# Performance work log

Hardware: AMD Instinct MI355X
Metric: run time of the kernel (lower is better)

Reference implementation:

```python
import jax, jax.numpy as jnp
import numpy as np

B, S, HID = 1, 2048, 2048
NH = 16
QL, KVL = 1536, 512
DN, DR, DV = 128, 64, 128
DQ = DN + DR  # 192
IH, ID = 4, 128
TOPK = 1024
EPS = 1e-6
THETA = 10000.0


def rope_interleaved(x, cos, sin):
    # x: (b,s,h,d); cos/sin: (s,d//2); pairs are (x[...,2i], x[...,2i+1])
    xr = x[..., 0::2]
    xi = x[..., 1::2]
    c = cos[None, :, None, :]
    s = sin[None, :, None, :]
    yr = xr * c - xi * s
    yi = xr * s + xi * c
    return jnp.stack([yr, yi], axis=-1).reshape(x.shape)


def rope_noninterleaved(x, cos, sin):
    # rotate-half style: pairs are (x[...,i], x[...,i+d/2])
    d = x.shape[-1] // 2
    x1, x2 = x[..., :d], x[..., d:]
    c = cos[None, :, None, :]
    s = sin[None, :, None, :]
    return jnp.concatenate([x1 * c - x2 * s, x1 * s + x2 * c], axis=-1)


def rmsnorm(x, w):
    var = jnp.mean(x * x, axis=-1, keepdims=True)
    return w * (x * jax.lax.rsqrt(var + EPS))


def layernorm(x, g, b):
    mu = jnp.mean(x, axis=-1, keepdims=True)
    var = jnp.mean((x - mu) ** 2, axis=-1, keepdims=True)
    return (x - mu) * jax.lax.rsqrt(var + EPS) * g + b


def setup_inputs() -> dict:
    key = jax.random.key(0)
    ks = jax.random.split(key, 12)
    std = 0.02
    x = jax.random.normal(ks[0], (B, S, HID), jnp.float32)
    pos = jnp.arange(S, dtype=jnp.float32)
    inv_freq = THETA ** (-jnp.arange(0, DR, 2, dtype=jnp.float32) / DR)
    ang = pos[:, None] * inv_freq[None, :]  # (S, DR//2)
    cos, sin = jnp.cos(ang), jnp.sin(ang)
    mask = jnp.where(jnp.tril(jnp.ones((S, S), bool)), 0.0, -1e9).astype(jnp.float32)
    return {
        "x": x, "cos": cos, "sin": sin, "mask": mask,
        "Wq_a": jax.random.normal(ks[1], (HID, QL), jnp.float32) * std,
        "q_norm_w": jnp.ones((QL,), jnp.float32),
        "Wq_b": jax.random.normal(ks[2], (QL, NH * DQ), jnp.float32) * std,
        "Wkv_a": jax.random.normal(ks[3], (HID, KVL + DR), jnp.float32) * std,
        "kv_norm_w": jnp.ones((KVL,), jnp.float32),
        "Wkv_b": jax.random.normal(ks[4], (KVL, NH * (DN + DV)), jnp.float32) * std,
        "Wo": jax.random.normal(ks[5], (NH * DV, HID), jnp.float32) * std,
        "IWq_b": jax.random.normal(ks[6], (QL, IH * ID), jnp.float32) * std,
        "IWk": jax.random.normal(ks[7], (HID, ID), jnp.float32) * std,
        "Ik_norm_w": jnp.ones((ID,), jnp.float32),
        "Ik_norm_b": jnp.zeros((ID,), jnp.float32),
        "IWproj": jax.random.normal(ks[8], (HID, IH), jnp.float32) * std,
    }


def indexer(x, qr, cos, sin, mask, IWq_b, IWk, Ik_norm_w, Ik_norm_b, IWproj):
    b, s, _ = x.shape
    q = (qr @ IWq_b).reshape(b, s, IH, ID)
    q_pe, q_nope = q[..., :DR], q[..., DR:]
    q_pe = rope_noninterleaved(q_pe, cos, sin)
    q = jnp.concatenate([q_pe, q_nope], axis=-1)
    k = layernorm(x @ IWk, Ik_norm_w, Ik_norm_b)  # (b,s,ID)
    k_pe = rope_noninterleaved(k[:, :, None, :DR], cos, sin)[:, :, 0]
    k = jnp.concatenate([k_pe, k[..., DR:]], axis=-1)
    weights = (x @ IWproj) * (IH ** -0.5) * (ID ** -0.5)  # (b,s,IH)
    logits = jax.nn.relu(jnp.einsum('bthd,bsd->btsh', q, k))
    index_score = jnp.einsum('btsh,bth->bts', logits, weights)
    index_score = index_score + mask[None]
    k_top = min(TOPK, s)
    topk_idx = jax.lax.top_k(index_score, k_top)[1]  # (b,s,k)
    bi = jnp.arange(b)[:, None, None]
    si = jnp.arange(s)[None, :, None]
    index_mask = jnp.full((b, s, s), -1e9, jnp.float32).at[bi, si, topk_idx].set(0.0)
    return index_mask


def reference(x, cos, sin, mask, Wq_a, q_norm_w, Wq_b, Wkv_a, kv_norm_w, Wkv_b, Wo,
              IWq_b, IWk, Ik_norm_w, Ik_norm_b, IWproj):
    b, s, _ = x.shape
    qr = rmsnorm(x @ Wq_a, q_norm_w)  # (b,s,QL)
    q = (qr @ Wq_b).reshape(b, s, NH, DQ)
    q_nope, q_pe = q[..., :DN], q[..., DN:]
    q_pe = rope_interleaved(q_pe, cos, sin)
    q = jnp.concatenate([q_nope, q_pe], axis=-1)
    kv_full = x @ Wkv_a
    kv, k_pe = kv_full[..., :KVL], kv_full[..., KVL:]
    kv = rmsnorm(kv, kv_norm_w)
    k_pe = rope_interleaved(k_pe[:, :, None, :], cos, sin)  # (b,s,1,DR)
    kv_exp = (kv @ Wkv_b).reshape(b, s, NH, DN + DV)
    k_nope, v = kv_exp[..., :DN], kv_exp[..., DN:]
    k = jnp.concatenate([k_nope, jnp.broadcast_to(k_pe, (b, s, NH, DR))], axis=-1)
    scores = jnp.einsum('bshd,bthd->bsht', q, k) * (DQ ** -0.5)
    index_mask = indexer(x, qr, cos, sin, mask, IWq_b, IWk, Ik_norm_w, Ik_norm_b, IWproj)
    scores = scores + index_mask[:, :, None, :] + mask[None, :, None, :]
    probs = jax.nn.softmax(scores, axis=-1)
    out = jnp.einsum('bsht,bthd->bshd', probs, v).reshape(b, s, NH * DV)
    return out @ Wo
```

## Files before the change

kernel.cpp:

```cpp
#include <hip/hip_runtime.h>
#include <math.h>
#include <stdint.h>

#define S 2048
#define HID 2048
#define NH 16
#define QL 1536
#define KVL 512
#define DN 128
#define DR 64
#define DV 128
#define DQ 192
#define IH 4
#define ID 128
#define TOPK 1024

#define N1 2244
#define N2 3584

#define CDIV(a,b) (((a)+(b)-1)/(b))

typedef float f32x4 __attribute__((ext_vector_type(4)));
typedef short bf16x8 __attribute__((ext_vector_type(8)));

__device__ __forceinline__ ushort f2b(float f) {
    uint32_t u = __float_as_uint(f);
    u += 0x7fffu + ((u >> 16) & 1u);
    return (ushort)(u >> 16);
}

#define GLL16(g, l)                                                            \
    __builtin_amdgcn_global_load_lds(                                          \
        (const __attribute__((address_space(1))) void*)(g),                    \
        (__attribute__((address_space(3))) void*)(l), 16, 0, 0)

__global__ __launch_bounds__(256) void gemm_bt(const ushort* __restrict__ A,
                                               const ushort* __restrict__ BT,
                                               float* __restrict__ C,
                                               int M, int N, int K) {
    __shared__ ushort As[2][128 * 32];
    __shared__ ushort Bs[2][128 * 32];
    const int tid = threadIdx.x;
    const int w = tid >> 6, l = tid & 63;
    const int quad = l >> 4, lane = l & 15;
    const int row0 = blockIdx.y * 128, col0 = blockIdx.x * 128;
    const int wr = (w >> 1) * 64, wc = (w & 1) * 64;
    f32x4 acc[4][4];
#pragma unroll
    for (int i = 0; i < 4; i++)
#pragma unroll
        for (int j = 0; j < 4; j++) acc[i][j] = (f32x4)0.f;

    const int srow = w * 32 + (l >> 2);
    const int c8 = (l & 3) * 8;
    const ushort* pa0 = A + (size_t)(row0 + srow) * K + c8;
    const ushort* pa1 = A + (size_t)(row0 + srow + 16) * K + c8;
    int bn0 = col0 + srow;      if (bn0 > N - 1) bn0 = N - 1;
    int bn1 = col0 + srow + 16; if (bn1 > N - 1) bn1 = N - 1;
    const ushort* pb0 = BT + (size_t)bn0 * K + c8;
    const ushort* pb1 = BT + (size_t)bn1 * K + c8;
    const int soff = srow * 32 + c8;

    GLL16(pa0, &As[0][soff]);
    GLL16(pa1, &As[0][soff + 16 * 32]);
    GLL16(pb0, &Bs[0][soff]);
    GLL16(pb1, &Bs[0][soff + 16 * 32]);
    asm volatile("s_waitcnt vmcnt(0)" ::: "memory");
    __builtin_amdgcn_s_barrier();

    int cur = 0;
    for (int k0 = 0; k0 < K; k0 += 32) {
        const int nxt = cur ^ 1;
        if (k0 + 32 < K) {
            GLL16(pa0 + k0 + 32, &As[nxt][soff]);
            GLL16(pa1 + k0 + 32, &As[nxt][soff + 16 * 32]);
            GLL16(pb0 + k0 + 32, &Bs[nxt][soff]);
            GLL16(pb1 + k0 + 32, &Bs[nxt][soff + 16 * 32]);
        }
        bf16x8 af[4], bf[4];
#pragma unroll
        for (int mi = 0; mi < 4; mi++)
            af[mi] = *(const bf16x8*)(&As[cur][(wr + mi * 16 + lane) * 32 + quad * 8]);
#pragma unroll
        for (int ni = 0; ni < 4; ni++)
            bf[ni] = *(const bf16x8*)(&Bs[cur][(wc + ni * 16 + lane) * 32 + quad * 8]);
#pragma unroll
        for (int mi = 0; mi < 4; mi++)
#pragma unroll
            for (int ni = 0; ni < 4; ni++)
                acc[mi][ni] = __builtin_amdgcn_mfma_f32_16x16x32_bf16(af[mi], bf[ni], acc[mi][ni], 0, 0, 0);
        asm volatile("s_waitcnt vmcnt(0)" ::: "memory");
        __builtin_amdgcn_s_barrier();
        cur = nxt;
    }
#pragma unroll
    for (int mi = 0; mi < 4; mi++)
#pragma unroll
        for (int ni = 0; ni < 4; ni++)
#pragma unroll
            for (int r = 0; r < 4; r++) {
                int row = row0 + wr + mi * 16 + quad * 4 + r;
                int col = col0 + wc + ni * 16 + lane;
                if (col < N) C[(size_t)row * N + col] = acc[mi][ni][r];
            }
}

__global__ __launch_bounds__(256) void gemm_bt_h(const ushort* __restrict__ A,
                                                 const ushort* __restrict__ BT,
                                                 ushort* __restrict__ C,
                                                 int M, int N, int K) {
    __shared__ ushort As[2][128 * 32];
    __shared__ ushort Bs[2][128 * 32];
    const int tid = threadIdx.x;
    const int w = tid >> 6, l = tid & 63;
    const int quad = l >> 4, lane = l & 15;
    const int row0 = blockIdx.y * 128, col0 = blockIdx.x * 128;
    const int wr = (w >> 1) * 64, wc = (w & 1) * 64;
    f32x4 acc[4][4];
#pragma unroll
    for (int i = 0; i < 4; i++)
#pragma unroll
        for (int j = 0; j < 4; j++) acc[i][j] = (f32x4)0.f;

    const int srow = w * 32 + (l >> 2);
    const int c8 = (l & 3) * 8;
    const ushort* pa0 = A + (size_t)(row0 + srow) * K + c8;
    const ushort* pa1 = A + (size_t)(row0 + srow + 16) * K + c8;
    int bn0 = col0 + srow;      if (bn0 > N - 1) bn0 = N - 1;
    int bn1 = col0 + srow + 16; if (bn1 > N - 1) bn1 = N - 1;
    const ushort* pb0 = BT + (size_t)bn0 * K + c8;
    const ushort* pb1 = BT + (size_t)bn1 * K + c8;
    const int soff = srow * 32 + c8;

    GLL16(pa0, &As[0][soff]);
    GLL16(pa1, &As[0][soff + 16 * 32]);
    GLL16(pb0, &Bs[0][soff]);
    GLL16(pb1, &Bs[0][soff + 16 * 32]);
    asm volatile("s_waitcnt vmcnt(0)" ::: "memory");
    __builtin_amdgcn_s_barrier();

    int cur = 0;
    for (int k0 = 0; k0 < K; k0 += 32) {
        const int nxt = cur ^ 1;
        if (k0 + 32 < K) {
            GLL16(pa0 + k0 + 32, &As[nxt][soff]);
            GLL16(pa1 + k0 + 32, &As[nxt][soff + 16 * 32]);
            GLL16(pb0 + k0 + 32, &Bs[nxt][soff]);
            GLL16(pb1 + k0 + 32, &Bs[nxt][soff + 16 * 32]);
        }
        bf16x8 af[4], bf[4];
#pragma unroll
        for (int mi = 0; mi < 4; mi++)
            af[mi] = *(const bf16x8*)(&As[cur][(wr + mi * 16 + lane) * 32 + quad * 8]);
#pragma unroll
        for (int ni = 0; ni < 4; ni++)
            bf[ni] = *(const bf16x8*)(&Bs[cur][(wc + ni * 16 + lane) * 32 + quad * 8]);
#pragma unroll
        for (int mi = 0; mi < 4; mi++)
#pragma unroll
            for (int ni = 0; ni < 4; ni++)
                acc[mi][ni] = __builtin_amdgcn_mfma_f32_16x16x32_bf16(af[mi], bf[ni], acc[mi][ni], 0, 0, 0);
        asm volatile("s_waitcnt vmcnt(0)" ::: "memory");
        __builtin_amdgcn_s_barrier();
        cur = nxt;
    }
#pragma unroll
    for (int mi = 0; mi < 4; mi++)
#pragma unroll
        for (int ni = 0; ni < 4; ni++)
#pragma unroll
            for (int r = 0; r < 4; r++) {
                int row = row0 + wr + mi * 16 + quad * 4 + r;
                int col = col0 + wc + ni * 16 + lane;
                if (col < N) C[(size_t)row * N + col] = f2b(acc[mi][ni][r]);
            }
}

__device__ __forceinline__ void wtrans_body(const float* W, ushort* WT, int K, int N,
                                            int k0, int n0) {
    __shared__ float t[64][65];
    int rr = threadIdx.x >> 6, cc = threadIdx.x & 63;
#pragma unroll
    for (int p = 0; p < 16; p++) {
        int k = k0 + p * 4 + rr, n = n0 + cc;
        t[p * 4 + rr][cc] = (k < K && n < N) ? W[(size_t)k * N + n] : 0.f;
    }
    __syncthreads();
#pragma unroll
    for (int p = 0; p < 16; p++) {
        int n = n0 + p * 4 + rr, k = k0 + cc;
        if (n < N && k < K) WT[(size_t)n * K + k] = f2b(t[cc][p * 4 + rr]);
    }
}

__global__ __launch_bounds__(256) void wtrans(const float* __restrict__ W, ushort* __restrict__ WT,
                                              int K, int N) {
    wtrans_body(W, WT, K, N, blockIdx.x * 64, blockIdx.y * 64);
}

__global__ __launch_bounds__(256) void wtrans_c1(const float* __restrict__ W0, const float* __restrict__ W1,
                                                 const float* __restrict__ W2, const float* __restrict__ W3,
                                                 ushort* __restrict__ WT) {
    int yb = blockIdx.y;
    const float* W; int N; size_t off; int y;
    if (yb < 24)      { W = W0; N = 1536; off = 0;                      y = yb; }
    else if (yb < 33) { W = W1; N = 576;  off = (size_t)1536 * HID;     y = yb - 24; }
    else if (yb < 35) { W = W2; N = 128;  off = (size_t)2112 * HID;     y = yb - 33; }
    else              { W = W3; N = 4;    off = (size_t)2240 * HID;     y = yb - 35; }
    wtrans_body(W, WT + off, HID, N, blockIdx.x * 64, y * 64);
}

__global__ __launch_bounds__(256) void wtrans_c2(const float* __restrict__ W0, const float* __restrict__ W1,
                                                 ushort* __restrict__ WT) {
    int yb = blockIdx.y;
    const float* W; int N; size_t off; int y;
    if (yb < 48) { W = W0; N = 3072; off = 0;                  y = yb; }
    else         { W = W1; N = 512;  off = (size_t)3072 * QL;  y = yb - 48; }
    wtrans_body(W, WT + off, QL, N, blockIdx.x * 64, y * 64);
}

__global__ void cvt_bf16(const float* __restrict__ in, ushort* __restrict__ out) {
    int i = blockIdx.x * 256 + threadIdx.x;
    float4 v = *(const float4*)(in + (size_t)i * 4);
    uint32_t lo = (uint32_t)f2b(v.x) | ((uint32_t)f2b(v.y) << 16);
    uint32_t hi = (uint32_t)f2b(v.z) | ((uint32_t)f2b(v.w) << 16);
    *(uint2*)(out + (size_t)i * 4) = make_uint2(lo, hi);
}

__global__ __launch_bounds__(256) void post_c1(const float* __restrict__ C1,
                                               const float* __restrict__ qw,
                                               const float* __restrict__ kvw,
                                               const float* __restrict__ ikg,
                                               const float* __restrict__ ikb,
                                               const float* __restrict__ cosb,
                                               const float* __restrict__ sinb,
                                               ushort* __restrict__ qrb,
                                               ushort* __restrict__ kvnb,
                                               float* __restrict__ kpe,
                                               float* __restrict__ kiT) {
    const int t = blockIdx.x, tid = threadIdx.x;
    const float* row = C1 + (size_t)t * N1;
    __shared__ float red[256];
    __shared__ float kis[128];
    float ss = 0.f;
    for (int i = tid; i < 1536; i += 256) { float v = row[i]; ss += v * v; }
    red[tid] = ss; __syncthreads();
    for (int st = 128; st > 0; st >>= 1) { if (tid < st) red[tid] += red[tid + st]; __syncthreads(); }
    float sq = rsqrtf(red[0] / 1536.f + 1e-6f);
    __syncthreads();
    float s2 = 0.f;
    for (int i = tid; i < 512; i += 256) { float v = row[1536 + i]; s2 += v * v; }
    red[tid] = s2; __syncthreads();
    for (int st = 128; st > 0; st >>= 1) { if (tid < st) red[tid] += red[tid + st]; __syncthreads(); }
    float skv = rsqrtf(red[0] / 512.f + 1e-6f);
    __syncthreads();
    float kv_ = (tid < 128) ? row[2112 + tid] : 0.f;
    red[tid] = kv_; __syncthreads();
    for (int st = 128; st > 0; st >>= 1) { if (tid < st) red[tid] += red[tid + st]; __syncthreads(); }
    float mu = red[0] / 128.f;
    __syncthreads();
    red[tid] = kv_ * kv_; __syncthreads();
    for (int st = 128; st > 0; st >>= 1) { if (tid < st) red[tid] += red[tid + st]; __syncthreads(); }
    float var = red[0] / 128.f - mu * mu;
    for (int i = tid; i < 1536; i += 256) qrb[(size_t)t * QL + i] = f2b(row[i] * sq * qw[i]);
    for (int i = tid; i < 512; i += 256)  kvnb[(size_t)t * KVL + i] = f2b(row[1536 + i] * skv * kvw[i]);
    if (tid < 32) {
        float c = cosb[t * 32 + tid], s = sinb[t * 32 + tid];
        float xr = row[2048 + 2 * tid], xi = row[2048 + 2 * tid + 1];
        kpe[t * 64 + 2 * tid]     = xr * c - xi * s;
        kpe[t * 64 + 2 * tid + 1] = xr * s + xi * c;
    }
    if (tid < 128) kis[tid] = (kv_ - mu) * rsqrtf(var + 1e-6f) * ikg[tid] + ikb[tid];
    __syncthreads();
    if (tid < 128) {
        float outv;
        if (tid < 32) {
            float c = cosb[t * 32 + tid], s = sinb[t * 32 + tid];
            outv = kis[tid] * c - kis[tid + 32] * s;
        } else if (tid < 64) {
            int j = tid - 32;
            float c = cosb[t * 32 + j], s = sinb[t * 32 + j];
            outv = kis[j] * s + kis[tid] * c;
        } else {
            outv = kis[tid];
        }
        kiT[(size_t)tid * S + t] = outv;
    }
}

__global__ __launch_bounds__(256) void post_c2(float* __restrict__ C2,
                                               const float* __restrict__ cosb,
                                               const float* __restrict__ sinb,
                                               ushort* __restrict__ qb) {
    const int t = blockIdx.x, tid = threadIdx.x;
    __shared__ float cs[32], sn[32];
    if (tid < 32) { cs[tid] = cosb[t * 32 + tid]; sn[tid] = sinb[t * 32 + tid]; }
    __syncthreads();
    const float sc = 0.10412775370051047f;
    const float* src0 = C2 + (size_t)t * N2;
    for (int i = tid; i < NH * 96; i += 256) {
        int h = i / 96, p = i % 96;
        const float* src = src0 + h * 192;
        ushort* dst = qb + ((size_t)h * S + t) * 192;
        if (p < 64) {
            dst[2 * p]     = f2b(src[2 * p] * sc);
            dst[2 * p + 1] = f2b(src[2 * p + 1] * sc);
        } else {
            int j = p - 64;
            float c = cs[j], s = sn[j];
            float xr = src[128 + 2 * j], xi = src[128 + 2 * j + 1];
            dst[128 + 2 * j]     = f2b((xr * c - xi * s) * sc);
            dst[128 + 2 * j + 1] = f2b((xr * s + xi * c) * sc);
        }
    }
    if (tid < 128) {
        int h = tid >> 5, j = tid & 31;
        float* p = C2 + (size_t)t * N2 + 3072 + h * 128;
        float c = cs[j], s = sn[j];
        float x1 = p[j], x2 = p[j + 32];
        p[j] = x1 * c - x2 * s;
        p[j + 32] = x1 * s + x2 * c;
    }
}

__global__ __launch_bounds__(256) void pack_kv(const ushort* __restrict__ kvexp_h,
                                               const float* __restrict__ kpe,
                                               ushort* __restrict__ kb,
                                               ushort* __restrict__ vT) {
    __shared__ ushort t[64][136];
    const int s0 = blockIdx.x * 64, h = blockIdx.y, tid = threadIdx.x;
    const int row = tid >> 2, c = tid & 3;
    const ushort* src = kvexp_h + (size_t)(s0 + row) * 4096 + h * 256;
    ushort* kbr = kb + ((size_t)h * S + s0 + row) * 192;
#pragma unroll
    for (int i = 0; i < 4; i++) {
        int off = c * 32 + i * 8;
        *(uint4*)(kbr + off) = *(const uint4*)(src + off);
        *(uint4*)(&t[row][off]) = *(const uint4*)(src + 128 + off);
    }
    const float* kp = kpe + (size_t)(s0 + row) * 64 + c * 16;
#pragma unroll
    for (int i = 0; i < 16; i++) kbr[128 + c * 16 + i] = f2b(kp[i]);
    __syncthreads();
    const int d = tid >> 1, sh = (tid & 1) * 32;
    ushort* dst = vT + ((size_t)h * 128 + d) * S + s0 + sh;
#pragma unroll
    for (int i = 0; i < 32; i++) dst[i] = t[sh + i][d];
}

__global__ __launch_bounds__(256) void iscore4(const float* __restrict__ qi,
                                               const float* __restrict__ kiT,
                                               const float* __restrict__ iw,
                                               float* __restrict__ iscore) {
    int t = blockIdx.x;
    int s0 = blockIdx.y * 1024;
    if (s0 > t) return;
    int s = s0 + threadIdx.x * 4;
    __shared__ float qs[4 * ID];
    __shared__ float ws4[4];
    for (int i = threadIdx.x; i < 4 * ID; i += 256) qs[i] = qi[(size_t)t * N2 + i];
    if (threadIdx.x < 4) ws4[threadIdx.x] = iw[(size_t)t * N1 + threadIdx.x] * 0.04419417382415922f;
    __syncthreads();
    if (s > t) return;
    float a[4][4];
#pragma unroll
    for (int h = 0; h < 4; h++)
#pragma unroll
        for (int c = 0; c < 4; c++) a[h][c] = 0.f;
    for (int d = 0; d < ID; d++) {
        float4 kv = *(const float4*)(kiT + (size_t)d * S + s);
#pragma unroll
        for (int h = 0; h < 4; h++) {
            float qv = qs[h * ID + d];
            a[h][0] += qv * kv.x; a[h][1] += qv * kv.y;
            a[h][2] += qv * kv.z; a[h][3] += qv * kv.w;
        }
    }
#pragma unroll
    for (int c = 0; c < 4; c++) {
        if (s + c > t) break;
        float sc = fmaxf(a[0][c], 0.f) * ws4[0] + fmaxf(a[1][c], 0.f) * ws4[1] +
                   fmaxf(a[2][c], 0.f) * ws4[2] + fmaxf(a[3][c], 0.f) * ws4[3];
        iscore[(size_t)t * S + s + c] = sc;
    }
}

__device__ inline unsigned sortable_u32(float f) {
    unsigned u = __float_as_uint(f);
    return (u & 0x80000000u) ? ~u : (u | 0x80000000u);
}

__global__ __launch_bounds__(256) void topk_mask(const float* __restrict__ iscore,
                                                 uint32_t* __restrict__ msk) {
    int t = blockIdx.x, tid = threadIdx.x;
    uint32_t* mrow = msk + (size_t)t * 64;
    if (t < TOPK) {
        if (tid < 64) {
            int full = (t + 1) >> 5;
            uint32_t wv2 = (tid < full) ? 0xFFFFFFFFu : 0u;
            if (tid == full) { int rem = (t + 1) & 31; wv2 = rem ? ((1u << rem) - 1u) : 0u; }
            mrow[tid] = wv2;
        }
        return;
    }
    const float* row = iscore + (size_t)t * S;
    const int n = t + 1;
    const int wv = tid >> 6;
    __shared__ int hist[4][256];
    __shared__ int scan[256];
    __shared__ int bsel, ksel;
    __shared__ uint32_t bytes[256];

    int jb = tid * 8;
    float4 v0 = *(const float4*)(row + jb);
    float4 v1 = *(const float4*)(row + jb + 4);
    uint32_t lsu[8];
    {
        float vvv[8] = {v0.x, v0.y, v0.z, v0.w, v1.x, v1.y, v1.z, v1.w};
#pragma unroll
        for (int i = 0; i < 8; i++)
            lsu[i] = (jb + i < n) ? sortable_u32(vvv[i]) : 0u;
    }
    unsigned prefix = 0, prefmask = 0;
    int k = TOPK;
    for (int pass = 0; pass < 4; pass++) {
        int shift = 24 - pass * 8;
#pragma unroll
        for (int r = 0; r < 4; r++) hist[r][tid] = 0;
        __syncthreads();
#pragma unroll
        for (int i = 0; i < 8; i++) {
            uint32_t u = lsu[i];
            if ((u & prefmask) == prefix) atomicAdd(&hist[wv][(u >> shift) & 255], 1);
        }
        __syncthreads();
        int h = hist[0][tid] + hist[1][tid] + hist[2][tid] + hist[3][tid];
        scan[tid] = h; __syncthreads();
        for (int st = 1; st < 256; st <<= 1) {
            int a = scan[tid];
            int b = (tid + st < 256) ? scan[tid + st] : 0;
            __syncthreads();
            scan[tid] = a + b;
            __syncthreads();
        }
        int snext = (tid < 255) ? scan[tid + 1] : 0;
        if (scan[tid] >= k && snext < k) { bsel = tid; ksel = k - snext; }
        __syncthreads();
        prefix |= ((unsigned)bsel) << shift;
        prefmask |= 0xFFu << shift;
        k = ksel;
        __syncthreads();
    }
    const unsigned u_thr = prefix;
    const int need = k;
    uint32_t gtbits = 0, eqbits = 0;
    int eqcnt = 0;
#pragma unroll
    for (int i = 0; i < 8; i++) {
        uint32_t u = lsu[i];
        if (u > u_thr) gtbits |= 1u << i;
        else if (u == u_thr) { eqbits |= 1u << i; eqcnt++; }
    }
    scan[tid] = eqcnt; __syncthreads();
    for (int st = 1; st < 256; st <<= 1) {
        int a = scan[tid];
        int b = (tid >= st) ? scan[tid - st] : 0;
        __syncthreads();
        scan[tid] = a + b;
        __syncthreads();
    }
    int room = need - (scan[tid] - eqcnt);
    uint32_t keep = 0;
#pragma unroll
    for (int i = 0; i < 8; i++)
        if ((eqbits >> i) & 1u) { if (room > 0) { keep |= 1u << i; room--; } }
    bytes[tid] = gtbits | keep;
    __syncthreads();
    if (tid < 64)
        mrow[tid] = bytes[tid * 4] | (bytes[tid * 4 + 1] << 8) |
                    (bytes[tid * 4 + 2] << 16) | (bytes[tid * 4 + 3] << 24);
}

__global__ __launch_bounds__(256, 2) void fattn6(const ushort* __restrict__ qb,
                                                 const ushort* __restrict__ kb,
                                                 const ushort* __restrict__ vT,
                                                 const uint32_t* __restrict__ msk,
                                                 float* __restrict__ Opart,
                                                 float* __restrict__ mlbuf) {
    __shared__ ushort Ks[24 * 512];
    __shared__ ushort Vs[16 * 512];
    __shared__ ushort Pm[4][16 * 72];
    const int tid = threadIdx.x;
    const int w = tid >> 6, l = tid & 63, quad = l >> 4, lane = l & 15;
    const int b = blockIdx.x;
    const int r8 = b & 7, j = b >> 3;
    const int h = r8 + 8 * (j & 1);
    const int idx = j >> 1;
    const int pair = idx & 15, part = idx >> 4;
    const int ta = pair, tb = 31 - pair, nA = ta + 1;
    const int vlo = part * 11, vhi = vlo + 11;
    const int qa0 = ta * 64, qb0 = tb * 64;

    bf16x8 qfa[6], qfb[6];
    {
        const ushort* qpa = qb + ((size_t)h * S + qa0 + w * 16 + lane) * 192;
        const ushort* qpb = qb + ((size_t)h * S + qb0 + w * 16 + lane) * 192;
#pragma unroll
        for (int ks = 0; ks < 6; ks++) {
            qfa[ks] = *(const bf16x8*)(qpa + ks * 32 + quad * 8);
            qfb[ks] = *(const bf16x8*)(qpb + ks * 32 + quad * 8);
        }
    }
    f32x4 oa[8], ob[8];
#pragma unroll
    for (int i = 0; i < 8; i++) { oa[i] = (f32x4)0.f; ob[i] = (f32x4)0.f; }
    float ma[4], la[4], mb[4], lb[4];
#pragma unroll
    for (int r = 0; r < 4; r++) { ma[r] = -1e30f; la[r] = 0.f; mb[r] = -1e30f; lb[r] = 0.f; }

    ushort* pw = &Pm[w][0];
    const ushort* kbase = kb + (size_t)h * S * 192;
    const ushort* vbase = vT + (size_t)h * 128 * S;

    for (int kt = 0; kt <= tb; kt++) {
        const int idxB = (kt <= ta) ? 2 * kt : kt + nA;
        const int hasA = (kt <= ta);
        const int idxA = 2 * kt + 1;
        const bool doB = (idxB >= vlo && idxB < vhi);
        const bool doA = hasA && (idxA >= vlo && idxA < vhi);
        if (!(doA || doB)) continue;
        const int s0 = kt * 64;
        __syncthreads();
#pragma unroll
        for (int ii = 0; ii < 6; ii++) {
            const int i = w * 6 + ii;
            const int ks = i >> 2, kq = i & 3;
            const ushort* src = kbase + (size_t)(s0 + kq * 16 + lane) * 192 + ks * 32 + quad * 8;
            GLL16(src, Ks + i * 512 + l * 8);
        }
#pragma unroll
        for (int ii = 0; ii < 4; ii++) {
            const int i = w * 4 + ii;
            const int k2 = i >> 3, nt = i & 7;
            const ushort* src = vbase + (size_t)(nt * 16 + lane) * S + s0 + k2 * 32 + quad * 8;
            GLL16(src, Vs + i * 512 + l * 8);
        }
        __syncthreads();

#pragma unroll
        for (int pass = 0; pass < 2; pass++) {
            if (pass == 0 && !doA) continue;
            if (pass == 1 && !doB) continue;
            const bf16x8* qf = (pass == 0) ? qfa : qfb;
            f32x4* oacc      = (pass == 0) ? oa : ob;
            float* mm        = (pass == 0) ? ma : mb;
            float* ll        = (pass == 0) ? la : lb;
            const int q0t    = (pass == 0) ? qa0 : qb0;

            f32x4 sc[4];
#pragma unroll
            for (int kq = 0; kq < 4; kq++) {
                sc[kq] = (f32x4)0.f;
#pragma unroll
                for (int ks = 0; ks < 6; ks++) {
                    bf16x8 bfr = *(const bf16x8*)(Ks + (ks * 4 + kq) * 512 + quad * 128 + lane * 8);
                    sc[kq] = __builtin_amdgcn_mfma_f32_16x16x32_bf16(qf[ks], bfr, sc[kq], 0, 0, 0);
                }
            }
            uint32_t w0[4], w1[4];
            {
                const int rowbase = q0t + w * 16 + quad * 4;
#pragma unroll
                for (int r = 0; r < 4; r++) {
                    const uint32_t* mp = msk + (size_t)(rowbase + r) * 64 + (s0 >> 5);
                    w0[r] = mp[0]; w1[r] = mp[1];
                }
            }
            float vmax[4] = {-1e30f, -1e30f, -1e30f, -1e30f};
#pragma unroll
            for (int kq = 0; kq < 4; kq++) {
                const int sh = (kq & 1) * 16 + lane;
#pragma unroll
                for (int r = 0; r < 4; r++) {
                    uint32_t word = (kq < 2) ? w0[r] : w1[r];
                    float v = ((word >> sh) & 1u) ? sc[kq][r] : -1e30f;
                    sc[kq][r] = v;
                    vmax[r] = fmaxf(vmax[r], v);
                }
            }
#pragma unroll
            for (int off = 1; off < 16; off <<= 1)
#pragma unroll
                for (int r = 0; r < 4; r++)
                    vmax[r] = fmaxf(vmax[r], __shfl_xor(vmax[r], off, 64));
            float alpha[4], psum[4];
#pragma unroll
            for (int r = 0; r < 4; r++) {
                float mnew = fmaxf(mm[r], vmax[r]);
                alpha[r] = exp2f(mm[r] - mnew);
                mm[r] = mnew;
                psum[r] = 0.f;
            }
#pragma unroll
            for (int kq = 0; kq < 4; kq++)
#pragma unroll
                for (int r = 0; r < 4; r++) {
                    float v = sc[kq][r];
                    float e = (v < -1e29f) ? 0.f : exp2f(v - mm[r]);
                    psum[r] += e;
                    pw[(quad * 4 + r) * 72 + kq * 16 + lane] = f2b(e);
                }
#pragma unroll
            for (int off = 1; off < 16; off <<= 1)
#pragma unroll
                for (int r = 0; r < 4; r++)
                    psum[r] += __shfl_xor(psum[r], off, 64);
#pragma unroll
            for (int r = 0; r < 4; r++) ll[r] = ll[r] * alpha[r] + psum[r];

            bf16x8 pfr[2];
#pragma unroll
            for (int k2 = 0; k2 < 2; k2++)
                pfr[k2] = *(const bf16x8*)(pw + lane * 72 + k2 * 32 + quad * 8);
#pragma unroll
            for (int nt = 0; nt < 8; nt++) {
#pragma unroll
                for (int r = 0; r < 4; r++) oacc[nt][r] *= alpha[r];
#pragma unroll
                for (int k2 = 0; k2 < 2; k2++) {
                    bf16x8 vfr = *(const bf16x8*)(Vs + ((k2 * 8 + nt) * 4 + quad) * 128 + lane * 8);
                    oacc[nt] = __builtin_amdgcn_mfma_f32_16x16x32_bf16(pfr[k2], vfr, oacc[nt], 0, 0, 0);
                }
            }
        }
    }
#pragma unroll
    for (int pass = 0; pass < 2; pass++) {
        const f32x4* oacc = (pass == 0) ? oa : ob;
        const float* mm   = (pass == 0) ? ma : mb;
        const float* ll   = (pass == 0) ? la : lb;
        const int qt      = (pass == 0) ? ta : tb;
        float* Op = Opart + (size_t)((qt * 16 + h) * 3 + part) * (64 * 128);
        float* mlp = mlbuf + (size_t)((qt * 16 + h) * 3 + part) * 128;
#pragma unroll
        for (int nt = 0; nt < 8; nt++)
#pragma unroll
            for (int r = 0; r < 4; r++)
                Op[(w * 16 + quad * 4 + r) * 128 + nt * 16 + lane] = oacc[nt][r];
        if (lane == 0) {
#pragma unroll
            for (int r = 0; r < 4; r++) {
                mlp[(w * 16 + quad * 4 + r) * 2 + 0] = mm[r];
                mlp[(w * 16 + quad * 4 + r) * 2 + 1] = ll[r];
            }
        }
    }
}

__global__ __launch_bounds__(256) void attn_combine(const float* __restrict__ Opart,
                                                    const float* __restrict__ mlbuf,
                                                    ushort* __restrict__ attn_b) {
    const int qt = blockIdx.x, h = blockIdx.y, tid = threadIdx.x;
    const size_t base = ((size_t)qt * 16 + h) * 3;
    const float* Op0 = Opart + base * 8192;
    const float* Op1 = Op0 + 8192;
    const float* Op2 = Op1 + 8192;
    const float* ml0 = mlbuf + base * 128;
    const float* ml1 = ml0 + 128;
    const float* ml2 = ml1 + 128;
#pragma unroll
    for (int i = 0; i < 32; i++) {
        int id = tid + i * 256;
        int row = id >> 7, d = id & 127;
        float m0 = ml0[row * 2], l0 = ml0[row * 2 + 1];
        float m1 = ml1[row * 2], l1 = ml1[row * 2 + 1];
        float m2 = ml2[row * 2], l2 = ml2[row * 2 + 1];
        float m = fmaxf(fmaxf(m0, m1), m2);
        float e0 = exp2f(m0 - m), e1 = exp2f(m1 - m), e2 = exp2f(m2 - m);
        float linv = 1.f / (l0 * e0 + l1 * e1 + l2 * e2);
        float v = (Op0[id] * e0 + Op1[id] * e1 + Op2[id] * e2) * linv;
        attn_b[(size_t)(qt * 64 + row) * 2048 + h * 128 + d] = f2b(v);
    }
}

extern "C" void kernel_launch(void* const* d_in, const int* in_sizes, int n_in,
                              void* d_out, int out_size, void* d_ws, size_t ws_size,
                              hipStream_t stream) {
    const float* x        = (const float*)d_in[0];
    const float* cosb     = (const float*)d_in[1];
    const float* sinb     = (const float*)d_in[2];
    const float* Wq_a     = (const float*)d_in[4];
    const float* q_norm_w = (const float*)d_in[5];
    const float* Wq_b     = (const float*)d_in[6];
    const float* Wkv_a    = (const float*)d_in[7];
    const float* kv_norm_w= (const float*)d_in[8];
    const float* Wkv_b    = (const float*)d_in[9];
    const float* Wo       = (const float*)d_in[10];
    const float* IWq_b    = (const float*)d_in[11];
    const float* IWk      = (const float*)d_in[12];
    const float* Ik_norm_w= (const float*)d_in[13];
    const float* Ik_norm_b= (const float*)d_in[14];
    const float* IWproj   = (const float*)d_in[15];
    float* out = (float*)d_out;

    char* ws = (char*)d_ws;
    size_t o = 0;
    auto take = [&](size_t b) { char* p = ws + o; o += (b + 255) & ~(size_t)255; return p; };
    ushort* xb     = (ushort*)take((size_t)S * HID * 2);
    ushort* qrb    = (ushort*)take((size_t)S * QL * 2);
    ushort* qb     = (ushort*)take((size_t)NH * S * DQ * 2);
    ushort* kvnb   = (ushort*)take((size_t)S * KVL * 2);
    float*  kpe    = (float*)take((size_t)S * DR * 4);
    ushort* kb     = (ushort*)take((size_t)NH * S * DQ * 2);
    ushort* vT     = (ushort*)take((size_t)NH * DV * S * 2);
    uint32_t* msk  = (uint32_t*)take((size_t)S * 64 * 4);
    float*  mlbuf  = (float*)take((size_t)32 * 16 * 3 * 64 * 2 * 4);
    ushort* WTp    = (ushort*)take((size_t)N2 * QL * 2);
    float*  C1     = (float*)take((size_t)S * N1 * 4);
    char*   big    = take((size_t)32 * 16 * 3 * 8192 * 4 + 1024);
    ushort* kvexp_h= (ushort*)take((size_t)S * 4096 * 2);
    float*  kiT    = (float*)take((size_t)128 * S * 4);
    char*   poolb  = take((size_t)16777216);

    float* C2     = (float*)big;
    float* Opart  = (float*)big;
    float* iscore = (float*)poolb;
    ushort* attn_b = (ushort*)poolb;

    cvt_bf16<<<(S * HID) / 1024, 256, 0, stream>>>(x, xb);

    wtrans_c1<<<dim3(32, 36), 256, 0, stream>>>(Wq_a, Wkv_a, IWk, IWproj, WTp);
    gemm_bt<<<dim3(CDIV(N1, 128), S / 128), 256, 0, stream>>>(xb, WTp, C1, S, N1, HID);
    post_c1<<<S, 256, 0, stream>>>(C1, q_norm_w, kv_norm_w, Ik_norm_w, Ik_norm_b,
                                   cosb, sinb, qrb, kvnb, kpe, kiT);

    wtrans_c2<<<dim3(24, 56), 256, 0, stream>>>(Wq_b, IWq_b, WTp);
    gemm_bt<<<dim3(N2 / 128, S / 128), 256, 0, stream>>>(qrb, WTp, C2, S, N2, QL);
    post_c2<<<S, 256, 0, stream>>>(C2, cosb, sinb, qb);

    wtrans<<<dim3(8, 64), 256, 0, stream>>>(Wkv_b, WTp, KVL, NH * (DN + DV));
    gemm_bt_h<<<dim3(32, S / 128), 256, 0, stream>>>(kvnb, WTp, kvexp_h, S, NH * (DN + DV), KVL);
    pack_kv<<<dim3(S / 64, NH), 256, 0, stream>>>(kvexp_h, kpe, kb, vT);

    iscore4<<<dim3(S, S / 1024), 256, 0, stream>>>(C2 + 3072, kiT, C1 + 2240, iscore);
    topk_mask<<<S, 256, 0, stream>>>(iscore, msk);

    fattn6<<<768, 256, 0, stream>>>(qb, kb, vT, msk, Opart, mlbuf);
    attn_combine<<<dim3(32, 16), 256, 0, stream>>>(Opart, mlbuf, attn_b);

    wtrans<<<dim3(32, 32), 256, 0, stream>>>(Wo, WTp, NH * DV, HID);
    gemm_bt<<<dim3(HID / 128, S / 128), 256, 0, stream>>>(attn_b, WTp, out, S, HID, NH * DV);

    (void)in_sizes; (void)n_in; (void)out_size; (void)ws_size; (void)o;
}
```

Baseline: 514.9 us.

## Load K/V fragments directly from global memory and defer row-sum reduction

The attention kernel stops staging K and V tiles through shared memory behind two block barriers per key tile. Each wave now reads its MFMA B-operand fragments straight from global memory. The cross-lane shuffle reduction of the softmax row sums moves out of the inner loop to a single pass after all tiles, which works because the per-row rescale factor is uniform across lanes. This removes the barriers and LDS traffic, but each of the four waves now fetches the full K/V tile on its own, raising cache traffic and exposing global-load latency directly to the MFMA chain.

```diff
diff --git a/kernel.cpp b/kernel.cpp
--- a/kernel.cpp
+++ b/kernel.cpp
@@ -481,14 +481,12 @@
                     (bytes[tid * 4 + 2] << 16) | (bytes[tid * 4 + 3] << 24);
 }
 
-__global__ __launch_bounds__(256, 2) void fattn6(const ushort* __restrict__ qb,
+__global__ __launch_bounds__(256, 2) void fattn7(const ushort* __restrict__ qb,
                                                  const ushort* __restrict__ kb,
                                                  const ushort* __restrict__ vT,
                                                  const uint32_t* __restrict__ msk,
                                                  float* __restrict__ Opart,
                                                  float* __restrict__ mlbuf) {
-    __shared__ ushort Ks[24 * 512];
-    __shared__ ushort Vs[16 * 512];
     __shared__ ushort Pm[4][16 * 72];
     const int tid = threadIdx.x;
     const int w = tid >> 6, l = tid & 63, quad = l >> 4, lane = l & 15;
@@ -530,22 +528,6 @@
         const bool doA = hasA && (idxA >= vlo && idxA < vhi);
         if (!(doA || doB)) continue;
         const int s0 = kt * 64;
-        __syncthreads();
-#pragma unroll
-        for (int ii = 0; ii < 6; ii++) {
-            const int i = w * 6 + ii;
-            const int ks = i >> 2, kq = i & 3;
-            const ushort* src = kbase + (size_t)(s0 + kq * 16 + lane) * 192 + ks * 32 + quad * 8;
-            GLL16(src, Ks + i * 512 + l * 8);
-        }
-#pragma unroll
-        for (int ii = 0; ii < 4; ii++) {
-            const int i = w * 4 + ii;
-            const int k2 = i >> 3, nt = i & 7;
-            const ushort* src = vbase + (size_t)(nt * 16 + lane) * S + s0 + k2 * 32 + quad * 8;
-            GLL16(src, Vs + i * 512 + l * 8);
-        }
-        __syncthreads();
 
 #pragma unroll
         for (int pass = 0; pass < 2; pass++) {
@@ -557,13 +539,14 @@
             float* ll        = (pass == 0) ? la : lb;
             const int q0t    = (pass == 0) ? qa0 : qb0;
 
+            const ushort* krow = kbase + (size_t)(s0 + lane) * 192 + quad * 8;
             f32x4 sc[4];
 #pragma unroll
             for (int kq = 0; kq < 4; kq++) {
                 sc[kq] = (f32x4)0.f;
 #pragma unroll
                 for (int ks = 0; ks < 6; ks++) {
-                    bf16x8 bfr = *(const bf16x8*)(Ks + (ks * 4 + kq) * 512 + quad * 128 + lane * 8);
+                    bf16x8 bfr = *(const bf16x8*)(krow + (size_t)(kq * 16) * 192 + ks * 32);
                     sc[kq] = __builtin_amdgcn_mfma_f32_16x16x32_bf16(qf[ks], bfr, sc[kq], 0, 0, 0);
                 }
             }
@@ -611,29 +594,32 @@
                     pw[(quad * 4 + r) * 72 + kq * 16 + lane] = f2b(e);
                 }
 #pragma unroll
-            for (int off = 1; off < 16; off <<= 1)
-#pragma unroll
-                for (int r = 0; r < 4; r++)
-                    psum[r] += __shfl_xor(psum[r], off, 64);
-#pragma unroll
             for (int r = 0; r < 4; r++) ll[r] = ll[r] * alpha[r] + psum[r];
 
             bf16x8 pfr[2];
 #pragma unroll
             for (int k2 = 0; k2 < 2; k2++)
                 pfr[k2] = *(const bf16x8*)(pw + lane * 72 + k2 * 32 + quad * 8);
+            const ushort* vrow = vbase + (size_t)lane * S + s0 + quad * 8;
 #pragma unroll
             for (int nt = 0; nt < 8; nt++) {
 #pragma unroll
                 for (int r = 0; r < 4; r++) oacc[nt][r] *= alpha[r];
 #pragma unroll
                 for (int k2 = 0; k2 < 2; k2++) {
-                    bf16x8 vfr = *(const bf16x8*)(Vs + ((k2 * 8 + nt) * 4 + quad) * 128 + lane * 8);
+                    bf16x8 vfr = *(const bf16x8*)(vrow + (size_t)(nt * 16) * S + k2 * 32);
                     oacc[nt] = __builtin_amdgcn_mfma_f32_16x16x32_bf16(pfr[k2], vfr, oacc[nt], 0, 0, 0);
                 }
             }
         }
     }
+#pragma unroll
+    for (int off = 1; off < 16; off <<= 1)
+#pragma unroll
+        for (int r = 0; r < 4; r++) {
+            la[r] += __shfl_xor(la[r], off, 64);
+            lb[r] += __shfl_xor(lb[r], off, 64);
+        }
 #pragma unroll
     for (int pass = 0; pass < 2; pass++) {
         const f32x4* oacc = (pass == 0) ? oa : ob;
@@ -745,7 +731,7 @@
     iscore4<<<dim3(S, S / 1024), 256, 0, stream>>>(C2 + 3072, kiT, C1 + 2240, iscore);
     topk_mask<<<S, 256, 0, stream>>>(iscore, msk);
 
-    fattn6<<<768, 256, 0, stream>>>(qb, kb, vT, msk, Opart, mlbuf);
+    fattn7<<<768, 256, 0, stream>>>(qb, kb, vT, msk, Opart, mlbuf);
     attn_combine<<<dim3(32, 16), 256, 0, stream>>>(Opart, mlbuf, attn_b);
 
     wtrans<<<dim3(32, 32), 256, 0, stream>>>(Wo, WTp, NH * DV, HID);
```

Result: slower. 590.7 us (+14.7%).

## Register-prefetch next K/V tile, bound kt range, defer row-sum reduction in attention

Applied to the files above, without the earlier changes.

Rewrites the attention kernel's K/V loading: the global loads now go into registers for the next tile while the current tile is computed, replacing the direct global-to-LDS loads. The kt loop range is computed up front, so the per-iteration skip test is dropped. Per-tile row-sum shuffles are moved to one reduction after the loop, which is valid because alpha is uniform across lanes. s_setprio is raised around the MFMA blocks. The register staging adds 40 VGPRs, which may hurt occupancy under launch_bounds(256,2).

```diff
diff --git a/kernel.cpp b/kernel.cpp
--- a/kernel.cpp
+++ b/kernel.cpp
@@ -481,7 +481,7 @@
                     (bytes[tid * 4 + 2] << 16) | (bytes[tid * 4 + 3] << 24);
 }
 
-__global__ __launch_bounds__(256, 2) void fattn6(const ushort* __restrict__ qb,
+__global__ __launch_bounds__(256, 2) void fattn8(const ushort* __restrict__ qb,
                                                  const ushort* __restrict__ kb,
                                                  const ushort* __restrict__ vT,
                                                  const uint32_t* __restrict__ msk,
@@ -501,6 +501,9 @@
     const int vlo = part * 11, vhi = vlo + 11;
     const int qa0 = ta * 64, qb0 = tb * 64;
 
+    const int kt_lo = (vlo <= 2 * ta + 1) ? (vlo >> 1) : (vlo - nA);
+    const int kt_hi = (vhi - 1 <= 2 * ta + 1) ? ((vhi - 1) >> 1) : (vhi - 1 - nA);
+
     bf16x8 qfa[6], qfb[6];
     {
         const ushort* qpa = qb + ((size_t)h * S + qa0 + w * 16 + lane) * 192;
@@ -522,30 +525,55 @@
     const ushort* kbase = kb + (size_t)h * S * 192;
     const ushort* vbase = vT + (size_t)h * 128 * S;
 
-    for (int kt = 0; kt <= tb; kt++) {
+    uint4 stg[10];
+    {
+        const int s0 = kt_lo * 64;
+#pragma unroll
+        for (int ii = 0; ii < 6; ii++) {
+            const int i = w * 6 + ii, ks = i >> 2, kq = i & 3;
+            stg[ii] = *(const uint4*)(kbase + (size_t)(s0 + kq * 16 + lane) * 192 + ks * 32 + quad * 8);
+        }
+#pragma unroll
+        for (int ii = 0; ii < 4; ii++) {
+            const int i = w * 4 + ii, k2 = i >> 3, nt = i & 7;
+            stg[6 + ii] = *(const uint4*)(vbase + (size_t)(nt * 16 + lane) * S + s0 + k2 * 32 + quad * 8);
+        }
+    }
+
+    for (int kt = kt_lo; kt <= kt_hi; kt++) {
         const int idxB = (kt <= ta) ? 2 * kt : kt + nA;
         const int hasA = (kt <= ta);
         const int idxA = 2 * kt + 1;
         const bool doB = (idxB >= vlo && idxB < vhi);
         const bool doA = hasA && (idxA >= vlo && idxA < vhi);
-        if (!(doA || doB)) continue;
         const int s0 = kt * 64;
+
         __syncthreads();
 #pragma unroll
         for (int ii = 0; ii < 6; ii++) {
             const int i = w * 6 + ii;
-            const int ks = i >> 2, kq = i & 3;
-            const ushort* src = kbase + (size_t)(s0 + kq * 16 + lane) * 192 + ks * 32 + quad * 8;
-            GLL16(src, Ks + i * 512 + l * 8);
+            *(uint4*)(Ks + i * 512 + l * 8) = stg[ii];
         }
 #pragma unroll
         for (int ii = 0; ii < 4; ii++) {
             const int i = w * 4 + ii;
-            const int k2 = i >> 3, nt = i & 7;
-            const ushort* src = vbase + (size_t)(nt * 16 + lane) * S + s0 + k2 * 32 + quad * 8;
-            GLL16(src, Vs + i * 512 + l * 8);
+            *(uint4*)(Vs + i * 512 + l * 8) = stg[6 + ii];
         }
         __syncthreads();
+
+        if (kt < kt_hi) {
+            const int s0n = s0 + 64;
+#pragma unroll
+            for (int ii = 0; ii < 6; ii++) {
+                const int i = w * 6 + ii, ks = i >> 2, kq = i & 3;
+                stg[ii] = *(const uint4*)(kbase + (size_t)(s0n + kq * 16 + lane) * 192 + ks * 32 + quad * 8);
+            }
+#pragma unroll
+            for (int ii = 0; ii < 4; ii++) {
+                const int i = w * 4 + ii, k2 = i >> 3, nt = i & 7;
+                stg[6 + ii] = *(const uint4*)(vbase + (size_t)(nt * 16 + lane) * S + s0n + k2 * 32 + quad * 8);
+            }
+        }
 
 #pragma unroll
         for (int pass = 0; pass < 2; pass++) {
@@ -558,6 +586,7 @@
             const int q0t    = (pass == 0) ? qa0 : qb0;
 
             f32x4 sc[4];
+            __builtin_amdgcn_s_setprio(1);
 #pragma unroll
             for (int kq = 0; kq < 4; kq++) {
                 sc[kq] = (f32x4)0.f;
@@ -567,6 +596,7 @@
                     sc[kq] = __builtin_amdgcn_mfma_f32_16x16x32_bf16(qf[ks], bfr, sc[kq], 0, 0, 0);
                 }
             }
+            __builtin_amdgcn_s_setprio(0);
             uint32_t w0[4], w1[4];
             {
                 const int rowbase = q0t + w * 16 + quad * 4;
@@ -611,17 +641,13 @@
                     pw[(quad * 4 + r) * 72 + kq * 16 + lane] = f2b(e);
                 }
 #pragma unroll
-            for (int off = 1; off < 16; off <<= 1)
-#pragma unroll
-                for (int r = 0; r < 4; r++)
-                    psum[r] += __shfl_xor(psum[r], off, 64);
-#pragma unroll
             for (int r = 0; r < 4; r++) ll[r] = ll[r] * alpha[r] + psum[r];
 
             bf16x8 pfr[2];
 #pragma unroll
             for (int k2 = 0; k2 < 2; k2++)
                 pfr[k2] = *(const bf16x8*)(pw + lane * 72 + k2 * 32 + quad * 8);
+            __builtin_amdgcn_s_setprio(1);
 #pragma unroll
             for (int nt = 0; nt < 8; nt++) {
 #pragma unroll
@@ -632,8 +658,16 @@
                     oacc[nt] = __builtin_amdgcn_mfma_f32_16x16x32_bf16(pfr[k2], vfr, oacc[nt], 0, 0, 0);
                 }
             }
-        }
-    }
+            __builtin_amdgcn_s_setprio(0);
+        }
+    }
+#pragma unroll
+    for (int off = 1; off < 16; off <<= 1)
+#pragma unroll
+        for (int r = 0; r < 4; r++) {
+            la[r] += __shfl_xor(la[r], off, 64);
+            lb[r] += __shfl_xor(lb[r], off, 64);
+        }
 #pragma unroll
     for (int pass = 0; pass < 2; pass++) {
         const f32x4* oacc = (pass == 0) ? oa : ob;
@@ -745,7 +779,7 @@
     iscore4<<<dim3(S, S / 1024), 256, 0, stream>>>(C2 + 3072, kiT, C1 + 2240, iscore);
     topk_mask<<<S, 256, 0, stream>>>(iscore, msk);
 
-    fattn6<<<768, 256, 0, stream>>>(qb, kb, vT, msk, Opart, mlbuf);
+    fattn8<<<768, 256, 0, stream>>>(qb, kb, vT, msk, Opart, mlbuf);
     attn_combine<<<dim3(32, 16), 256, 0, stream>>>(Opart, mlbuf, attn_b);
 
     wtrans<<<dim3(32, 32), 256, 0, stream>>>(Wo, WTp, NH * DV, HID);
```

Result: slower. 563.3 us (+9.4%).

## Triple-buffer GEMM loads and defer attention row-sum reduction with MFMA priority

Applied to the files above, without the earlier changes.

Both bf16 GEMM kernels move from a double-buffered to a triple-buffered LDS pipeline. Loads run two k-tiles ahead, and the wait is relaxed to vmcnt(4) so one tile's loads can stay in flight across the barrier. In the attention kernel, the per-iteration cross-lane shuffle reduction of the softmax row sum moves to a single reduction after the loop. This is valid because the row max is already uniform across lanes, so each lane's partial sum is scaled by the same alpha. The MFMA sections are also wrapped in s_setprio to favour matrix issue across waves, at the cost of more LDS use in the GEMMs, which may reduce occupancy.

```diff
diff --git a/kernel.cpp b/kernel.cpp
--- a/kernel.cpp
+++ b/kernel.cpp
@@ -38,8 +38,8 @@
                                                const ushort* __restrict__ BT,
                                                float* __restrict__ C,
                                                int M, int N, int K) {
-    __shared__ ushort As[2][128 * 32];
-    __shared__ ushort Bs[2][128 * 32];
+    __shared__ ushort As[3][128 * 32];
+    __shared__ ushort Bs[3][128 * 32];
     const int tid = threadIdx.x;
     const int w = tid >> 6, l = tid & 63;
     const int quad = l >> 4, lane = l & 15;
@@ -60,22 +60,30 @@
     const ushort* pb0 = BT + (size_t)bn0 * K + c8;
     const ushort* pb1 = BT + (size_t)bn1 * K + c8;
     const int soff = srow * 32 + c8;
-
-    GLL16(pa0, &As[0][soff]);
-    GLL16(pa1, &As[0][soff + 16 * 32]);
-    GLL16(pb0, &Bs[0][soff]);
-    GLL16(pb1, &Bs[0][soff + 16 * 32]);
-    asm volatile("s_waitcnt vmcnt(0)" ::: "memory");
+    const int nt = K >> 5;
+
+#define STAGE_G(t, s)                                                          \
+    {                                                                          \
+        GLL16(pa0 + (t) * 32, &As[s][soff]);                                   \
+        GLL16(pa1 + (t) * 32, &As[s][soff + 16 * 32]);                         \
+        GLL16(pb0 + (t) * 32, &Bs[s][soff]);                                   \
+        GLL16(pb1 + (t) * 32, &Bs[s][soff + 16 * 32]);                         \
+    }
+
+    STAGE_G(0, 0);
+    if (nt > 1) {
+        STAGE_G(1, 1);
+        asm volatile("s_waitcnt vmcnt(4)" ::: "memory");
+    } else {
+        asm volatile("s_waitcnt vmcnt(0)" ::: "memory");
+    }
     __builtin_amdgcn_s_barrier();
 
     int cur = 0;
-    for (int k0 = 0; k0 < K; k0 += 32) {
-        const int nxt = cur ^ 1;
-        if (k0 + 32 < K) {
-            GLL16(pa0 + k0 + 32, &As[nxt][soff]);
-            GLL16(pa1 + k0 + 32, &As[nxt][soff + 16 * 32]);
-            GLL16(pb0 + k0 + 32, &Bs[nxt][soff]);
-            GLL16(pb1 + k0 + 32, &Bs[nxt][soff + 16 * 32]);
+    for (int t = 0; t < nt; ++t) {
+        if (t + 2 < nt) {
+            int pf = cur + 2; if (pf >= 3) pf -= 3;
+            STAGE_G(t + 2, pf);
         }
         bf16x8 af[4], bf[4];
 #pragma unroll
@@ -89,9 +97,10 @@
 #pragma unroll
             for (int ni = 0; ni < 4; ni++)
                 acc[mi][ni] = __builtin_amdgcn_mfma_f32_16x16x32_bf16(af[mi], bf[ni], acc[mi][ni], 0, 0, 0);
-        asm volatile("s_waitcnt vmcnt(0)" ::: "memory");
+        if (t + 2 < nt) asm volatile("s_waitcnt vmcnt(4)" ::: "memory");
+        else            asm volatile("s_waitcnt vmcnt(0)" ::: "memory");
         __builtin_amdgcn_s_barrier();
-        cur = nxt;
+        cur = cur + 1; if (cur == 3) cur = 0;
     }
 #pragma unroll
     for (int mi = 0; mi < 4; mi++)
@@ -109,8 +118,8 @@
                                                  const ushort* __restrict__ BT,
                                                  ushort* __restrict__ C,
                                                  int M, int N, int K) {
-    __shared__ ushort As[2][128 * 32];
-    __shared__ ushort Bs[2][128 * 32];
+    __shared__ ushort As[3][128 * 32];
+    __shared__ ushort Bs[3][128 * 32];
     const int tid = threadIdx.x;
     const int w = tid >> 6, l = tid & 63;
     const int quad = l >> 4, lane = l & 15;
@@ -131,22 +140,22 @@
     const ushort* pb0 = BT + (size_t)bn0 * K + c8;
     const ushort* pb1 = BT + (size_t)bn1 * K + c8;
     const int soff = srow * 32 + c8;
-
-    GLL16(pa0, &As[0][soff]);
-    GLL16(pa1, &As[0][soff + 16 * 32]);
-    GLL16(pb0, &Bs[0][soff]);
-    GLL16(pb1, &Bs[0][soff + 16 * 32]);
-    asm volatile("s_waitcnt vmcnt(0)" ::: "memory");
+    const int nt = K >> 5;
+
+    STAGE_G(0, 0);
+    if (nt > 1) {
+        STAGE_G(1, 1);
+        asm volatile("s_waitcnt vmcnt(4)" ::: "memory");
+    } else {
+        asm volatile("s_waitcnt vmcnt(0)" ::: "memory");
+    }
     __builtin_amdgcn_s_barrier();
 
     int cur = 0;
-    for (int k0 = 0; k0 < K; k0 += 32) {
-        const int nxt = cur ^ 1;
-        if (k0 + 32 < K) {
-            GLL16(pa0 + k0 + 32, &As[nxt][soff]);
-            GLL16(pa1 + k0 + 32, &As[nxt][soff + 16 * 32]);
-            GLL16(pb0 + k0 + 32, &Bs[nxt][soff]);
-            GLL16(pb1 + k0 + 32, &Bs[nxt][soff + 16 * 32]);
+    for (int t = 0; t < nt; ++t) {
+        if (t + 2 < nt) {
+            int pf = cur + 2; if (pf >= 3) pf -= 3;
+            STAGE_G(t + 2, pf);
         }
         bf16x8 af[4], bf[4];
 #pragma unroll
@@ -160,9 +169,10 @@
 #pragma unroll
             for (int ni = 0; ni < 4; ni++)
                 acc[mi][ni] = __builtin_amdgcn_mfma_f32_16x16x32_bf16(af[mi], bf[ni], acc[mi][ni], 0, 0, 0);
-        asm volatile("s_waitcnt vmcnt(0)" ::: "memory");
+        if (t + 2 < nt) asm volatile("s_waitcnt vmcnt(4)" ::: "memory");
+        else            asm volatile("s_waitcnt vmcnt(0)" ::: "memory");
         __builtin_amdgcn_s_barrier();
-        cur = nxt;
+        cur = cur + 1; if (cur == 3) cur = 0;
     }
 #pragma unroll
     for (int mi = 0; mi < 4; mi++)
@@ -481,7 +491,7 @@
                     (bytes[tid * 4 + 2] << 16) | (bytes[tid * 4 + 3] << 24);
 }
 
-__global__ __launch_bounds__(256, 2) void fattn6(const ushort* __restrict__ qb,
+__global__ __launch_bounds__(256, 2) void fattn9(const ushort* __restrict__ qb,
                                                  const ushort* __restrict__ kb,
                                                  const ushort* __restrict__ vT,
                                                  const uint32_t* __restrict__ msk,
@@ -558,6 +568,7 @@
             const int q0t    = (pass == 0) ? qa0 : qb0;
 
             f32x4 sc[4];
+            __builtin_amdgcn_s_setprio(1);
 #pragma unroll
             for (int kq = 0; kq < 4; kq++) {
                 sc[kq] = (f32x4)0.f;
@@ -567,6 +578,7 @@
                     sc[kq] = __builtin_amdgcn_mfma_f32_16x16x32_bf16(qf[ks], bfr, sc[kq], 0, 0, 0);
                 }
             }
+            __builtin_amdgcn_s_setprio(0);
             uint32_t w0[4], w1[4];
             {
                 const int rowbase = q0t + w * 16 + quad * 4;
@@ -611,17 +623,13 @@
                     pw[(quad * 4 + r) * 72 + kq * 16 + lane] = f2b(e);
                 }
 #pragma unroll
-            for (int off = 1; off < 16; off <<= 1)
-#pragma unroll
-                for (int r = 0; r < 4; r++)
-                    psum[r] += __shfl_xor(psum[r], off, 64);
-#pragma unroll
             for (int r = 0; r < 4; r++) ll[r] = ll[r] * alpha[r] + psum[r];
 
             bf16x8 pfr[2];
 #pragma unroll
             for (int k2 = 0; k2 < 2; k2++)
                 pfr[k2] = *(const bf16x8*)(pw + lane * 72 + k2 * 32 + quad * 8);
+            __builtin_amdgcn_s_setprio(1);
 #pragma unroll
             for (int nt = 0; nt < 8; nt++) {
 #pragma unroll
@@ -632,8 +640,16 @@
                     oacc[nt] = __builtin_amdgcn_mfma_f32_16x16x32_bf16(pfr[k2], vfr, oacc[nt], 0, 0, 0);
                 }
             }
-        }
-    }
+            __builtin_amdgcn_s_setprio(0);
+        }
+    }
+#pragma unroll
+    for (int off = 1; off < 16; off <<= 1)
+#pragma unroll
+        for (int r = 0; r < 4; r++) {
+            la[r] += __shfl_xor(la[r], off, 64);
+            lb[r] += __shfl_xor(lb[r], off, 64);
+        }
 #pragma unroll
     for (int pass = 0; pass < 2; pass++) {
         const f32x4* oacc = (pass == 0) ? oa : ob;
@@ -745,7 +761,7 @@
     iscore4<<<dim3(S, S / 1024), 256, 0, stream>>>(C2 + 3072, kiT, C1 + 2240, iscore);
     topk_mask<<<S, 256, 0, stream>>>(iscore, msk);
 
-    fattn6<<<768, 256, 0, stream>>>(qb, kb, vT, msk, Opart, mlbuf);
+    fattn9<<<768, 256, 0, stream>>>(qb, kb, vT, msk, Opart, mlbuf);
     attn_combine<<<dim3(32, 16), 256, 0, stream>>>(Opart, mlbuf, attn_b);
 
     wtrans<<<dim3(32, 32), 256, 0, stream>>>(Wo, WTp, NH * DV, HID);
```

Result: slower. 532.9 us (+3.5%).
